# Kernel tuning notes

Hardware: AMD Instinct MI355X
Metric: run time of the kernel (lower is better)

The kernel has to match this reference:

```python
import jax, jax.numpy as jnp
import numpy as np


def setup_inputs() -> dict:
    key = jax.random.key(0)
    T, B, E, F = 128, 4, 10000, 16
    x = jax.random.normal(key, (T, B, E, F), dtype=jnp.float32)
    return {"x": x, "dummy_index": 0}


def reference(x, dummy_index):
    # x: [time, batch, element, feature]
    d = dummy_index
    # f: all features except the time column -> [T, B, E, F-1]
    f = jnp.concatenate([x[..., :d], x[..., d + 1:]], axis=-1)
    # t: the time coordinate column -> [T, B, E, 1]
    t = x[..., d:d + 1]
    # _diff: reflect-pad left by 1 (pad value = t[1]) then negate the pad,
    # so dt[0] = t[0] - (-t[1]) = t[0] + t[1], dt[i] = t[i] - t[i-1] for i >= 1
    dt0 = t[0] + t[1]                 # [B, E, 1]
    dt_rest = t[1:] - t[:-1]          # [T-1, B, E, 1]
    dt = jnp.concatenate([dt0[None], dt_rest], axis=0)  # [T, B, E, 1]
    # trapezoid-like accumulation: multiply, prefix-sum over time, activation
    integrated = jnp.cumsum(f * dt, axis=0)  # [T, B, E, F-1]
    return jnp.tanh(integrated)
```

## Files before the change

### kernel.cpp

```cpp
#include <hip/hip_runtime.h>


#define TT   128
#define X4_T 160000
#define O_T4 150000

__device__ __forceinline__ float fast_tanh(float x) {
  float e = __expf(2.0f * x);
  return 1.0f - __fdividef(2.0f, e + 1.0f);
}

__device__ __forceinline__ float quad_bcast0(float v) {
  return __int_as_float(
      __builtin_amdgcn_mov_dpp(__float_as_int(v), 0, 0xf, 0xf, true));
}

__global__ __launch_bounds__(256) void integ_kernel(const float* __restrict__ x,
                                                    float* __restrict__ out) {
  __shared__ __align__(16) float stage[4][240];

  const int tid  = threadIdx.x;
  const int gid  = blockIdx.x * 256 + tid;
  const int idx  = gid >> 2;
  const int sub  = gid & 3;
  const int wid  = tid >> 6;
  const int lane = tid & 63;
  const int g    = lane >> 2;

  const float4* xv = reinterpret_cast<const float4*>(x) + ((size_t)idx * 4 + sub);

  float* lw = &stage[wid][0] + (g * 15 + 4 * sub - 1);
  const float4* ls = reinterpret_cast<const float4*>(&stage[wid][0]) + lane;
  const int gbase = blockIdx.x * 64 + wid * 16;
  float4* op = reinterpret_cast<float4*>(out + (size_t)gbase * 15) + lane;

  float4 v   = xv[0];
  float4 vn1 = xv[(size_t)X4_T];
  float4 vn2 = xv[(size_t)2 * X4_T];

  float t0 = quad_bcast0(v.x);
  float t1 = quad_bcast0(vn1.x);
  float dt = t0 + t1;
  float a0 = v.x * dt;
  float a1 = v.y * dt;
  float a2 = v.z * dt;
  float a3 = v.w * dt;

  if (sub) lw[0] = fast_tanh(a0);
  lw[1] = fast_tanh(a1);
  lw[2] = fast_tanh(a2);
  lw[3] = fast_tanh(a3);
  asm volatile("s_waitcnt lgkmcnt(0)" ::: "memory");
  if (lane < 60) op[0] = *ls;

  float tprev = t0;
  v = vn1;
  vn1 = vn2;

#pragma unroll 4
  for (int t = 1; t < TT; ++t) {
    int tn = (t + 2 < TT) ? t + 2 : TT - 1;
    vn2 = xv[(size_t)tn * X4_T];

    float tc = quad_bcast0(v.x);
    dt = tc - tprev;
    a0 = fmaf(v.x, dt, a0);
    a1 = fmaf(v.y, dt, a1);
    a2 = fmaf(v.z, dt, a2);
    a3 = fmaf(v.w, dt, a3);

    if (sub) lw[0] = fast_tanh(a0);
    lw[1] = fast_tanh(a1);
    lw[2] = fast_tanh(a2);
    lw[3] = fast_tanh(a3);
    asm volatile("s_waitcnt lgkmcnt(0)" ::: "memory");
    if (lane < 60) op[(size_t)t * O_T4] = *ls;

    tprev = tc;
    v = vn1;
    vn1 = vn2;
  }
}

extern "C" void kernel_launch(void* const* d_in, const int* in_sizes, int n_in,
                              void* d_out, int out_size, void* d_ws, size_t ws_size,
                              hipStream_t stream) {
  const float* x = (const float*)d_in[0];
  float* out = (float*)d_out;
  integ_kernel<<<dim3(625), dim3(256), 0, stream>>>(x, out);
}
```

Baseline: 511.7 us.

## Split each element across eight lanes with float2 loads and deeper prefetch

Result: no change. 519.6 us (+1.5%).

```diff
diff --git a/kernel.cpp b/kernel.cpp
--- a/kernel.cpp
+++ b/kernel.cpp
@@ -1,84 +1,76 @@
 #include <hip/hip_runtime.h>
 
 
-#define TT   128
-#define X4_T 160000
-#define O_T4 150000
+#define TT    128
+#define X2_T  320000
+#define O_T4  150000
 
 __device__ __forceinline__ float fast_tanh(float x) {
   float e = __expf(2.0f * x);
   return 1.0f - __fdividef(2.0f, e + 1.0f);
 }
 
-__device__ __forceinline__ float quad_bcast0(float v) {
-  return __int_as_float(
-      __builtin_amdgcn_mov_dpp(__float_as_int(v), 0, 0xf, 0xf, true));
+__device__ __forceinline__ float oct_bcast0(float v) {
+  return __int_as_float(__builtin_amdgcn_ds_swizzle(__float_as_int(v), 0x18));
 }
 
 __global__ __launch_bounds__(256) void integ_kernel(const float* __restrict__ x,
                                                     float* __restrict__ out) {
-  __shared__ __align__(16) float stage[4][240];
+  __shared__ __align__(16) float stage[4][120];
 
   const int tid  = threadIdx.x;
   const int gid  = blockIdx.x * 256 + tid;
-  const int idx  = gid >> 2;
-  const int sub  = gid & 3;
+  const int idx  = gid >> 3;
+  const int sub  = gid & 7;
   const int wid  = tid >> 6;
   const int lane = tid & 63;
-  const int g    = lane >> 2;
+  const int g    = lane >> 3;
 
-  const float4* xv = reinterpret_cast<const float4*>(x) + ((size_t)idx * 4 + sub);
+  const float2* xv = reinterpret_cast<const float2*>(x) + ((size_t)idx * 8 + sub);
 
-  float* lw = &stage[wid][0] + (g * 15 + 4 * sub - 1);
+  float* sw = &stage[wid][0] + (g * 15 + 2 * sub);
   const float4* ls = reinterpret_cast<const float4*>(&stage[wid][0]) + lane;
-  const int gbase = blockIdx.x * 64 + wid * 16;
+  const int gbase = blockIdx.x * 32 + wid * 8;
   float4* op = reinterpret_cast<float4*>(out + (size_t)gbase * 15) + lane;
 
-  float4 v   = xv[0];
-  float4 vn1 = xv[(size_t)X4_T];
-  float4 vn2 = xv[(size_t)2 * X4_T];
+  float2 v0 = xv[0];
+  float2 v1 = xv[(size_t)X2_T];
+  float2 v2 = xv[(size_t)2 * X2_T];
+  float2 v3 = xv[(size_t)3 * X2_T];
 
-  float t0 = quad_bcast0(v.x);
-  float t1 = quad_bcast0(vn1.x);
+  float t0 = oct_bcast0(v0.x);
+  float t1 = oct_bcast0(v1.x);
   float dt = t0 + t1;
-  float a0 = v.x * dt;
-  float a1 = v.y * dt;
-  float a2 = v.z * dt;
-  float a3 = v.w * dt;
+  float a0 = v0.x * dt;
+  float a1 = v0.y * dt;
 
-  if (sub) lw[0] = fast_tanh(a0);
-  lw[1] = fast_tanh(a1);
-  lw[2] = fast_tanh(a2);
-  lw[3] = fast_tanh(a3);
-  asm volatile("s_waitcnt lgkmcnt(0)" ::: "memory");
-  if (lane < 60) op[0] = *ls;
+  if (sub) sw[-1] = fast_tanh(a0);
+  sw[0] = fast_tanh(a1);
+  __builtin_amdgcn_wave_barrier();
+  if (lane < 30) op[0] = *ls;
+  __builtin_amdgcn_wave_barrier();
 
   float tprev = t0;
-  v = vn1;
-  vn1 = vn2;
+  float2 cur = v1, n1 = v2, n2 = v3;
 
 #pragma unroll 4
   for (int t = 1; t < TT; ++t) {
-    int tn = (t + 2 < TT) ? t + 2 : TT - 1;
-    vn2 = xv[(size_t)tn * X4_T];
+    int tn = (t + 3 < TT) ? t + 3 : TT - 1;
+    float2 n3 = xv[(size_t)tn * X2_T];
 
-    float tc = quad_bcast0(v.x);
+    float tc = oct_bcast0(cur.x);
     dt = tc - tprev;
-    a0 = fmaf(v.x, dt, a0);
-    a1 = fmaf(v.y, dt, a1);
-    a2 = fmaf(v.z, dt, a2);
-    a3 = fmaf(v.w, dt, a3);
+    a0 = fmaf(cur.x, dt, a0);
+    a1 = fmaf(cur.y, dt, a1);
 
-    if (sub) lw[0] = fast_tanh(a0);
-    lw[1] = fast_tanh(a1);
-    lw[2] = fast_tanh(a2);
-    lw[3] = fast_tanh(a3);
-    asm volatile("s_waitcnt lgkmcnt(0)" ::: "memory");
-    if (lane < 60) op[(size_t)t * O_T4] = *ls;
+    if (sub) sw[-1] = fast_tanh(a0);
+    sw[0] = fast_tanh(a1);
+    __builtin_amdgcn_wave_barrier();
+    if (lane < 30) op[(size_t)t * O_T4] = *ls;
+    __builtin_amdgcn_wave_barrier();
 
     tprev = tc;
-    v = vn1;
-    vn1 = vn2;
+    cur = n1; n1 = n2; n2 = n3;
   }
 }
 
@@ -87,5 +79,5 @@
                               hipStream_t stream) {
   const float* x = (const float*)d_in[0];
   float* out = (float*)d_out;
-  integ_kernel<<<dim3(625), dim3(256), 0, stream>>>(x, out);
+  integ_kernel<<<dim3(1250), dim3(256), 0, stream>>>(x, out);
 }
```
